# Optimization experiments

Hardware: AMD Instinct MI355X
Metric: run time of the kernel (lower is better)

Reference implementation:

```python
import jax, jax.numpy as jnp
import numpy as np

B, S, I, H, F1, C = 1024, 512, 50, 64, 32, 2


def setup_inputs() -> dict:
    key = jax.random.key(0)
    ks = jax.random.split(key, 9)
    s_ih = 1.0 / np.sqrt(H)
    return {
        "x": jax.random.normal(ks[0], (B, S, I), dtype=jnp.float32),
        # PyTorch LSTM params, gate order (i, f, g, o) stacked along dim 0
        "W_ih": jax.random.uniform(ks[1], (4 * H, I), jnp.float32, -s_ih, s_ih),
        "W_hh": jax.random.uniform(ks[2], (4 * H, H), jnp.float32, -s_ih, s_ih),
        "b_ih": jax.random.uniform(ks[3], (4 * H,), jnp.float32, -s_ih, s_ih),
        "b_hh": jax.random.uniform(ks[4], (4 * H,), jnp.float32, -s_ih, s_ih),
        "W1": jax.random.uniform(ks[5], (F1, H), jnp.float32, -s_ih, s_ih),
        "b1": jax.random.uniform(ks[6], (F1,), jnp.float32, -s_ih, s_ih),
        "W2": jax.random.uniform(ks[7], (C, F1), jnp.float32, -1.0 / np.sqrt(F1), 1.0 / np.sqrt(F1)),
        "b2": jax.random.uniform(ks[8], (C,), jnp.float32, -1.0 / np.sqrt(F1), 1.0 / np.sqrt(F1)),
    }


def _lstm_last(x, W_ih, W_hh, b_ih, b_hh):
    # Precompute input contribution for all timesteps in one big GEMM: [B,S,4H]
    xg = jnp.einsum("bsi,gi->bsg", x, W_ih) + b_ih + b_hh
    Bn = x.shape[0]
    Hn = W_hh.shape[1]
    h0 = jnp.zeros((Bn, Hn), dtype=x.dtype)
    c0 = jnp.zeros((Bn, Hn), dtype=x.dtype)

    def step(carry, xt):
        h, c = carry
        g = xt + h @ W_hh.T  # [B,4H]
        i_g, f_g, g_g, o_g = jnp.split(g, 4, axis=-1)
        i_g = jax.nn.sigmoid(i_g)
        f_g = jax.nn.sigmoid(f_g)
        g_g = jnp.tanh(g_g)
        o_g = jax.nn.sigmoid(o_g)
        c_new = f_g * c + i_g * g_g
        h_new = o_g * jnp.tanh(c_new)
        return (h_new, c_new), None

    (h_last, _), _ = jax.lax.scan(step, (h0, c0), xg.transpose(1, 0, 2))
    return h_last  # == out[:, -1, :]


def reference(x, W_ih, W_hh, b_ih, b_hh, W1, b1, W2, b2):
    last_out = _lstm_last(x, W_ih, W_hh, b_ih, b_hh)
    # Dropout is identity in eval mode (deterministic reference)
    h = jax.nn.relu(last_out @ W1.T + b1)
    return h @ W2.T + b2  # [B, num_classes]
```

## Files before the change

kernel.cpp:

```cpp
#include <hip/hip_runtime.h>
#include <math.h>


#define S_LEN  512
#define I_DIM  50
#define H_DIM  64
#define BB     2
#define TC     16
#define NCH    (S_LEN / TC)
#define KROW   40
#define XROW   72
#define XSHALF (BB * TC * XROW)
#define NXE    (BB * TC * I_DIM)
#define F1_DIM 32
#define C_DIM  2

typedef __attribute__((ext_vector_type(8))) _Float16 f16x8;
typedef __attribute__((ext_vector_type(4))) float    f32x4;

__device__ __forceinline__ float fast_rcp(float x) { return __builtin_amdgcn_rcpf(x); }
__device__ __forceinline__ float sigm(float v) { return fast_rcp(1.0f + __expf(-v)); }
__device__ __forceinline__ float tanh_fast(float v) {
    return 1.0f - 2.0f * fast_rcp(__expf(2.0f * v) + 1.0f);
}

#define MFMA16(A, B, C) __builtin_amdgcn_mfma_f32_16x16x32_f16(A, B, C, 0, 0, 0)

#define BAR() do { asm volatile("s_waitcnt lgkmcnt(0)" ::: "memory"); \
                   __builtin_amdgcn_s_barrier(); } while (0)

__global__ __launch_bounds__(512, 4)
void lstm_mfma(const float* __restrict__ x,
               const float* __restrict__ W_ih, const float* __restrict__ W_hh,
               const float* __restrict__ b_ih, const float* __restrict__ b_hh,
               const float* __restrict__ W1,  const float* __restrict__ b1,
               const float* __restrict__ W2,  const float* __restrict__ b2,
               float* __restrict__ out)
{
    __shared__ __align__(16) _Float16 Hst[2][2][16][KROW];
    __shared__ __align__(16) _Float16 Xs[2][BB * TC][XROW];
    __shared__ __align__(16) float    XGb[2][TC][BB][H_DIM][4];
    __shared__ float f1buf[BB][F1_DIM];

    const int u  = threadIdx.x;
    const int w  = u >> 6;
    const int l  = u & 63;
    const int c  = l & 15;
    const int hk = l >> 4;
    const int b0 = blockIdx.x * BB;
    const bool is_scan = (w < 4);
    const int q  = w & 3;
    const f32x4 Z4 = {0.f, 0.f, 0.f, 0.f};

    f16x8 f0h, f1h, f2h, f3h, f4h, f5h, f6h, f7h;
    float bs0 = 0.f, bs1 = 0.f, bs2 = 0.f, bs3 = 0.f;
    float cst = 0.0f;

    f16x8 ga0, ga1;
    f32x4 G0, G1, G2, G3;

    const float *xp0=x,*xp1=x,*xp2=x,*xp3=x,*xp4=x,*xp5=x,*xp6=x;
    int  ld0=0,ld1=0,ld2=0,ld3=0,ld4=0,ld5=0,ld6=0;
    bool v0=false,v1=false,v2=false,v3=false,v4=false,v5=false,v6=false;

    {
        const int base = is_scan ? (16 * w + c) : (16 * q + c);
#define LDF(NM, G, KT) { \
        _Float16 tmp[8]; \
        _Pragma("unroll") \
        for (int j = 0; j < 8; ++j) { \
            const int kq = hk * 8 + j; \
            if (is_scan) { \
                tmp[j] = (_Float16)W_hh[(G * H_DIM + base) * H_DIM + (KT) * 32 + kq]; \
            } else { \
                const int kk = (KT) * 32 + kq; \
                tmp[j] = (kk < I_DIM) ? (_Float16)W_ih[(G * H_DIM + base) * I_DIM + kk] \
                                      : (_Float16)0.0f; \
            } \
        } \
        NM = *(const f16x8*)tmp; }
        LDF(f0h, 0, 0) LDF(f1h, 0, 1)
        LDF(f2h, 1, 0) LDF(f3h, 1, 1)
        LDF(f4h, 2, 0) LDF(f5h, 2, 1)
        LDF(f6h, 3, 0) LDF(f7h, 3, 1)
#undef LDF
        if (!is_scan) {
            bs0 = b_ih[0 * H_DIM + base] + b_hh[0 * H_DIM + base];
            bs1 = b_ih[1 * H_DIM + base] + b_hh[1 * H_DIM + base];
            bs2 = b_ih[2 * H_DIM + base] + b_hh[2 * H_DIM + base];
            bs3 = b_ih[3 * H_DIM + base] + b_hh[3 * H_DIM + base];

            const int ug = u - 256;
#define PRE(E) { const int idx = ug + (E) * 256; if (idx < NXE) { \
            const int bb_ = idx / (TC * I_DIM); \
            const int rm_ = idx - bb_ * (TC * I_DIM); \
            const int t_  = rm_ / I_DIM; \
            const int ii_ = rm_ - t_ * I_DIM; \
            xp##E = x + (size_t)(b0 + bb_) * (S_LEN * I_DIM) + t_ * I_DIM + ii_; \
            ld##E = (bb_ * TC + t_) * XROW + ii_; v##E = true; } }
            PRE(0) PRE(1) PRE(2) PRE(3) PRE(4) PRE(5) PRE(6)
#undef PRE
        }
    }

    for (int i = u; i < 1280; i += 512) ((unsigned*)Hst)[i] = 0u;
    for (int i = u; i < 2304; i += 512) ((unsigned*)Xs)[i]  = 0u;
    __syncthreads();

    if (!is_scan) {
#define STG(E, CH, BUF) if (v##E) { \
        const float t_ = xp##E[(size_t)(CH) * (TC * I_DIM)]; \
        *((_Float16*)Xs + (BUF) * XSHALF + ld##E) = (_Float16)t_; }
        STG(0,0,0) STG(1,0,0) STG(2,0,0) STG(3,0,0) STG(4,0,0) STG(5,0,0) STG(6,0,0)
        STG(0,1,1) STG(1,1,1) STG(2,1,1) STG(3,1,1) STG(4,1,1) STG(5,1,1) STG(6,1,1)
#undef STG
    }
    __syncthreads();

#define GPK(DB, MT, I) { f32x4 pk; \
    pk[0] = G0[I] + bs0; \
    pk[1] = G1[I] + bs1; \
    pk[2] = G2[I] + bs2; \
    pk[3] = G3[I] + bs3; \
    *(f32x4*)&XGb[DB][4 * hk + (I)][MT][16 * q + c][0] = pk; }

#define GQ0(SB, MT) { \
    ga0 = *(const f16x8*)&Xs[SB][(MT) * 16 + c][hk * 8]; \
    ga1 = *(const f16x8*)&Xs[SB][(MT) * 16 + c][32 + hk * 8]; \
    G0 = MFMA16(ga0, f0h, Z4); G0 = MFMA16(ga1, f1h, G0); }
#define GQ1() { \
    G1 = MFMA16(ga0, f2h, Z4); G1 = MFMA16(ga1, f3h, G1); }
#define GQ2() { \
    G2 = MFMA16(ga0, f4h, Z4); G2 = MFMA16(ga1, f5h, G2); }
#define GQ3(DB, MT) { \
    G3 = MFMA16(ga0, f6h, Z4); G3 = MFMA16(ga1, f7h, G3); \
    GPK(DB, MT, 0) GPK(DB, MT, 1) GPK(DB, MT, 2) GPK(DB, MT, 3) }

    if (!is_scan) {
        GQ0(0, 0) GQ1() GQ2() GQ3(0, 0)
        GQ0(0, 1) GQ1() GQ2() GQ3(0, 1)
    }
    __syncthreads();

#define SCAN_STEP(TT, CUR) { \
    const int p = (TT) & 1; \
    const f16x8 ah0 = *(const f16x8*)&Hst[p][0][c][hk * 8]; \
    const f16x8 ah1 = *(const f16x8*)&Hst[p][1][c][hk * 8]; \
    const int bq = hk & 1; \
    const f32x4 xg4 = *(const f32x4*)&XGb[CUR][TT][bq][16 * w + c][0]; \
    __builtin_amdgcn_s_setprio(1); \
    f32x4 A0 = MFMA16(ah0, f0h, ((f32x4){xg4[0], 0.f, 0.f, 0.f})); \
    A0 = MFMA16(ah1, f1h, A0); \
    f32x4 A1 = MFMA16(ah0, f2h, ((f32x4){xg4[1], 0.f, 0.f, 0.f})); \
    A1 = MFMA16(ah1, f3h, A1); \
    f32x4 A2 = MFMA16(ah0, f4h, ((f32x4){xg4[2], 0.f, 0.f, 0.f})); \
    A2 = MFMA16(ah1, f5h, A2); \
    f32x4 A3 = MFMA16(ah0, f6h, ((f32x4){xg4[3], 0.f, 0.f, 0.f})); \
    A3 = MFMA16(ah1, f7h, A3); \
    __builtin_amdgcn_s_setprio(0); \
    if (hk < 2) { \
        const float gi = sigm(A0[0]), gf = sigm(A1[0]); \
        const float gg = tanh_fast(A2[0]), go = sigm(A3[0]); \
        cst = fmaf(gf, cst, gi * gg); \
        const float hv = go * tanh_fast(cst); \
        const int uo = 16 * w + c; \
        Hst[p ^ 1][uo >> 5][4 * hk][uo & 31] = (_Float16)hv; \
    } }

#define XISS(E, CH2) if (v##E) xr##E = xp##E[(size_t)(CH2) * (TC * I_DIM)];
#define XCMT(E, BUF) if (v##E) *((_Float16*)Xs + (BUF) * XSHALF + ld##E) = (_Float16)xr##E;

    for (int ch = 0; ch < NCH; ++ch) {
        const int cur = ch & 1, nx = cur ^ 1;
        const bool cmp = (ch + 1 < NCH);
        const bool stg = (ch + 2 < NCH);
        float xr0=0,xr1=0,xr2=0,xr3=0,xr4=0,xr5=0,xr6=0;

        #pragma unroll
        for (int tt = 0; tt < TC; ++tt) {
            if (is_scan) {
                SCAN_STEP(tt, cur)
            } else {
                if (cmp && ((tt & 1) == 0)) {
                    const int mt = tt >> 3, gq = (tt >> 1) & 3;
                    if (gq == 0) { GQ0(nx, mt) }
                    if (gq == 1) { GQ1() }
                    if (gq == 2) { GQ2() }
                    if (gq == 3) { GQ3(nx, mt) }
                }
                if (stg) {
                    if (tt == 0) {
                        XISS(0, ch+2) XISS(1, ch+2) XISS(2, ch+2) XISS(3, ch+2)
                        XISS(4, ch+2) XISS(5, ch+2) XISS(6, ch+2)
                    }
                    if (tt == 6)  { XCMT(0, cur)  XCMT(1, cur) }
                    if (tt == 7)  { XCMT(2, cur)  XCMT(3, cur) }
                    if (tt == 9)  { XCMT(4, cur)  XCMT(5, cur) }
                    if (tt == 11) { XCMT(6, cur) }
                }
            }
            BAR();
        }
    }
#undef SCAN_STEP
#undef GQ0
#undef GQ1
#undef GQ2
#undef GQ3
#undef GPK
#undef XISS
#undef XCMT

    __syncthreads();

    if (u < BB * F1_DIM) {
        const int b = u >> 5, f = u & 31;
        float acc = b1[f];
        #pragma unroll
        for (int j = 0; j < H_DIM; ++j) {
            const float hj = (float)Hst[0][j >> 5][4 * b][j & 31];
            acc = fmaf(hj, W1[f * H_DIM + j], acc);
        }
        f1buf[b][f] = fmaxf(acc, 0.0f);
    }
    __syncthreads();
    if (u < BB * C_DIM) {
        const int b = u >> 1, cl = u & 1;
        float acc = b2[cl];
        #pragma unroll
        for (int f = 0; f < F1_DIM; ++f)
            acc = fmaf(f1buf[b][f], W2[cl * F1_DIM + f], acc);
        out[(size_t)(b0 + b) * C_DIM + cl] = acc;
    }
}

extern "C" void kernel_launch(void* const* d_in, const int* in_sizes, int n_in,
                              void* d_out, int out_size, void* d_ws, size_t ws_size,
                              hipStream_t stream) {
    const float* x   = (const float*)d_in[0];
    const float* Wih = (const float*)d_in[1];
    const float* Whh = (const float*)d_in[2];
    const float* bih = (const float*)d_in[3];
    const float* bhh = (const float*)d_in[4];
    const float* W1  = (const float*)d_in[5];
    const float* b1  = (const float*)d_in[6];
    const float* W2  = (const float*)d_in[7];
    const float* b2  = (const float*)d_in[8];
    float* out = (float*)d_out;

    hipLaunchKernelGGL(lstm_mfma, dim3(1024 / BB), dim3(512), 0, stream,
                       x, Wih, Whh, bih, bhh, W1, b1, W2, b2, out);
}
```

Baseline: 221.0 us.

## Merge scan and input-projection warps into one role, process four sequences per block

Removes the producer/consumer split where four warps ran the recurrence and four computed the input projection. Each of the four warps in a 256-thread block now does both, interleaving one input-projection MFMA pair per timestep with the recurrent step. Each block now handles four batch rows instead of two, so each scan MFMA row carries a real sequence. The goal is to halve the block count and use MFMA rows that previously held padding, at the cost of more registers per thread (both weight sets), lower occupancy, and a longer per-step critical path.

```diff
diff --git a/kernel.cpp b/kernel.cpp
--- a/kernel.cpp
+++ b/kernel.cpp
@@ -5,7 +5,7 @@
 #define S_LEN  512
 #define I_DIM  50
 #define H_DIM  64
-#define BB     2
+#define BB     4
 #define TC     16
 #define NCH    (S_LEN / TC)
 #define KROW   40
@@ -29,7 +29,7 @@
 #define BAR() do { asm volatile("s_waitcnt lgkmcnt(0)" ::: "memory"); \
                    __builtin_amdgcn_s_barrier(); } while (0)
 
-__global__ __launch_bounds__(512, 4)
+__global__ __launch_bounds__(256, 1)
 void lstm_mfma(const float* __restrict__ x,
                const float* __restrict__ W_ih, const float* __restrict__ W_hh,
                const float* __restrict__ b_ih, const float* __restrict__ b_hh,
@@ -48,73 +48,66 @@
     const int c  = l & 15;
     const int hk = l >> 4;
     const int b0 = blockIdx.x * BB;
-    const bool is_scan = (w < 4);
-    const int q  = w & 3;
+    const int base = 16 * w + c;
     const f32x4 Z4 = {0.f, 0.f, 0.f, 0.f};
 
-    f16x8 f0h, f1h, f2h, f3h, f4h, f5h, f6h, f7h;
-    float bs0 = 0.f, bs1 = 0.f, bs2 = 0.f, bs3 = 0.f;
+    f16x8 s00, s01, s10, s11, s20, s21, s30, s31;
+    f16x8 g00, g01, g10, g11, g20, g21, g30, g31;
+    {
+#define LDS_F(NM, G, KT) { _Float16 tmp[8]; \
+        _Pragma("unroll") for (int j = 0; j < 8; ++j) \
+            tmp[j] = (_Float16)W_hh[((G) * H_DIM + base) * H_DIM + (KT) * 32 + hk * 8 + j]; \
+        NM = *(const f16x8*)tmp; }
+#define LDG_F(NM, G, KT) { _Float16 tmp[8]; \
+        _Pragma("unroll") for (int j = 0; j < 8; ++j) { \
+            const int kk = (KT) * 32 + hk * 8 + j; \
+            tmp[j] = (kk < I_DIM) ? (_Float16)W_ih[((G) * H_DIM + base) * I_DIM + kk] \
+                                  : (_Float16)0.0f; } \
+        NM = *(const f16x8*)tmp; }
+        LDS_F(s00, 0, 0) LDS_F(s01, 0, 1) LDS_F(s10, 1, 0) LDS_F(s11, 1, 1)
+        LDS_F(s20, 2, 0) LDS_F(s21, 2, 1) LDS_F(s30, 3, 0) LDS_F(s31, 3, 1)
+        LDG_F(g00, 0, 0) LDG_F(g01, 0, 1) LDG_F(g10, 1, 0) LDG_F(g11, 1, 1)
+        LDG_F(g20, 2, 0) LDG_F(g21, 2, 1) LDG_F(g30, 3, 0) LDG_F(g31, 3, 1)
+#undef LDS_F
+#undef LDG_F
+    }
+    const float bs0 = b_ih[0 * H_DIM + base] + b_hh[0 * H_DIM + base];
+    const float bs1 = b_ih[1 * H_DIM + base] + b_hh[1 * H_DIM + base];
+    const float bs2 = b_ih[2 * H_DIM + base] + b_hh[2 * H_DIM + base];
+    const float bs3 = b_ih[3 * H_DIM + base] + b_hh[3 * H_DIM + base];
     float cst = 0.0f;
 
     f16x8 ga0, ga1;
     f32x4 G0, G1, G2, G3;
 
-    const float *xp0=x,*xp1=x,*xp2=x,*xp3=x,*xp4=x,*xp5=x,*xp6=x;
-    int  ld0=0,ld1=0,ld2=0,ld3=0,ld4=0,ld5=0,ld6=0;
-    bool v0=false,v1=false,v2=false,v3=false,v4=false,v5=false,v6=false;
-
-    {
-        const int base = is_scan ? (16 * w + c) : (16 * q + c);
-#define LDF(NM, G, KT) { \
-        _Float16 tmp[8]; \
-        _Pragma("unroll") \
-        for (int j = 0; j < 8; ++j) { \
-            const int kq = hk * 8 + j; \
-            if (is_scan) { \
-                tmp[j] = (_Float16)W_hh[(G * H_DIM + base) * H_DIM + (KT) * 32 + kq]; \
-            } else { \
-                const int kk = (KT) * 32 + kq; \
-                tmp[j] = (kk < I_DIM) ? (_Float16)W_ih[(G * H_DIM + base) * I_DIM + kk] \
-                                      : (_Float16)0.0f; \
-            } \
-        } \
-        NM = *(const f16x8*)tmp; }
-        LDF(f0h, 0, 0) LDF(f1h, 0, 1)
-        LDF(f2h, 1, 0) LDF(f3h, 1, 1)
-        LDF(f4h, 2, 0) LDF(f5h, 2, 1)
-        LDF(f6h, 3, 0) LDF(f7h, 3, 1)
-#undef LDF
-        if (!is_scan) {
-            bs0 = b_ih[0 * H_DIM + base] + b_hh[0 * H_DIM + base];
-            bs1 = b_ih[1 * H_DIM + base] + b_hh[1 * H_DIM + base];
-            bs2 = b_ih[2 * H_DIM + base] + b_hh[2 * H_DIM + base];
-            bs3 = b_ih[3 * H_DIM + base] + b_hh[3 * H_DIM + base];
-
-            const int ug = u - 256;
-#define PRE(E) { const int idx = ug + (E) * 256; if (idx < NXE) { \
-            const int bb_ = idx / (TC * I_DIM); \
-            const int rm_ = idx - bb_ * (TC * I_DIM); \
-            const int t_  = rm_ / I_DIM; \
-            const int ii_ = rm_ - t_ * I_DIM; \
-            xp##E = x + (size_t)(b0 + bb_) * (S_LEN * I_DIM) + t_ * I_DIM + ii_; \
-            ld##E = (bb_ * TC + t_) * XROW + ii_; v##E = true; } }
-            PRE(0) PRE(1) PRE(2) PRE(3) PRE(4) PRE(5) PRE(6)
+    const float *xp0=x,*xp1=x,*xp2=x,*xp3=x,*xp4=x,*xp5=x,*xp6=x,
+                *xp7=x,*xp8=x,*xp9=x,*xp10=x,*xp11=x,*xp12=x;
+    int  ld0=0,ld1=0,ld2=0,ld3=0,ld4=0,ld5=0,ld6=0,ld7=0,ld8=0,ld9=0,ld10=0,ld11=0,ld12=0;
+    bool v0=false,v1=false,v2=false,v3=false,v4=false,v5=false,v6=false,
+         v7=false,v8=false,v9=false,v10=false,v11=false,v12=false;
+#define PRE(E) { const int idx = u + (E) * 256; if (idx < NXE) { \
+        const int bb_ = idx / (TC * I_DIM); \
+        const int rm_ = idx - bb_ * (TC * I_DIM); \
+        const int t_  = rm_ / I_DIM; \
+        const int ii_ = rm_ - t_ * I_DIM; \
+        xp##E = x + (size_t)(b0 + bb_) * (S_LEN * I_DIM) + t_ * I_DIM + ii_; \
+        ld##E = (bb_ * TC + t_) * XROW + ii_; v##E = true; } }
+    PRE(0) PRE(1) PRE(2) PRE(3) PRE(4) PRE(5) PRE(6)
+    PRE(7) PRE(8) PRE(9) PRE(10) PRE(11) PRE(12)
 #undef PRE
-        }
-    }
-
-    for (int i = u; i < 1280; i += 512) ((unsigned*)Hst)[i] = 0u;
-    for (int i = u; i < 2304; i += 512) ((unsigned*)Xs)[i]  = 0u;
-    __syncthreads();
-
-    if (!is_scan) {
+
+    for (int i = u; i < 1280; i += 256) ((unsigned*)Hst)[i] = 0u;
+    for (int i = u; i < 4608; i += 256) ((unsigned*)Xs)[i]  = 0u;
+    __syncthreads();
+
 #define STG(E, CH, BUF) if (v##E) { \
-        const float t_ = xp##E[(size_t)(CH) * (TC * I_DIM)]; \
-        *((_Float16*)Xs + (BUF) * XSHALF + ld##E) = (_Float16)t_; }
-        STG(0,0,0) STG(1,0,0) STG(2,0,0) STG(3,0,0) STG(4,0,0) STG(5,0,0) STG(6,0,0)
-        STG(0,1,1) STG(1,1,1) STG(2,1,1) STG(3,1,1) STG(4,1,1) STG(5,1,1) STG(6,1,1)
+    const float t_ = xp##E[(size_t)(CH) * (TC * I_DIM)]; \
+    *((_Float16*)Xs + (BUF) * XSHALF + ld##E) = (_Float16)t_; }
+    STG(0,0,0) STG(1,0,0) STG(2,0,0) STG(3,0,0) STG(4,0,0) STG(5,0,0) STG(6,0,0)
+    STG(7,0,0) STG(8,0,0) STG(9,0,0) STG(10,0,0) STG(11,0,0) STG(12,0,0)
+    STG(0,1,1) STG(1,1,1) STG(2,1,1) STG(3,1,1) STG(4,1,1) STG(5,1,1) STG(6,1,1)
+    STG(7,1,1) STG(8,1,1) STG(9,1,1) STG(10,1,1) STG(11,1,1) STG(12,1,1)
 #undef STG
-    }
     __syncthreads();
 
 #define GPK(DB, MT, I) { f32x4 pk; \
@@ -122,50 +115,25 @@
     pk[1] = G1[I] + bs1; \
     pk[2] = G2[I] + bs2; \
     pk[3] = G3[I] + bs3; \
-    *(f32x4*)&XGb[DB][4 * hk + (I)][MT][16 * q + c][0] = pk; }
+    *(f32x4*)&XGb[DB][4 * hk + (I)][MT][base][0] = pk; }
 
 #define GQ0(SB, MT) { \
     ga0 = *(const f16x8*)&Xs[SB][(MT) * 16 + c][hk * 8]; \
     ga1 = *(const f16x8*)&Xs[SB][(MT) * 16 + c][32 + hk * 8]; \
-    G0 = MFMA16(ga0, f0h, Z4); G0 = MFMA16(ga1, f1h, G0); }
+    G0 = MFMA16(ga0, g00, Z4); G0 = MFMA16(ga1, g01, G0); }
 #define GQ1() { \
-    G1 = MFMA16(ga0, f2h, Z4); G1 = MFMA16(ga1, f3h, G1); }
+    G1 = MFMA16(ga0, g10, Z4); G1 = MFMA16(ga1, g11, G1); }
 #define GQ2() { \
-    G2 = MFMA16(ga0, f4h, Z4); G2 = MFMA16(ga1, f5h, G2); }
+    G2 = MFMA16(ga0, g20, Z4); G2 = MFMA16(ga1, g21, G2); }
 #define GQ3(DB, MT) { \
-    G3 = MFMA16(ga0, f6h, Z4); G3 = MFMA16(ga1, f7h, G3); \
+    G3 = MFMA16(ga0, g30, Z4); G3 = MFMA16(ga1, g31, G3); \
     GPK(DB, MT, 0) GPK(DB, MT, 1) GPK(DB, MT, 2) GPK(DB, MT, 3) }
 
-    if (!is_scan) {
-        GQ0(0, 0) GQ1() GQ2() GQ3(0, 0)
-        GQ0(0, 1) GQ1() GQ2() GQ3(0, 1)
-    }
-    __syncthreads();
-
-#define SCAN_STEP(TT, CUR) { \
-    const int p = (TT) & 1; \
-    const f16x8 ah0 = *(const f16x8*)&Hst[p][0][c][hk * 8]; \
-    const f16x8 ah1 = *(const f16x8*)&Hst[p][1][c][hk * 8]; \
-    const int bq = hk & 1; \
-    const f32x4 xg4 = *(const f32x4*)&XGb[CUR][TT][bq][16 * w + c][0]; \
-    __builtin_amdgcn_s_setprio(1); \
-    f32x4 A0 = MFMA16(ah0, f0h, ((f32x4){xg4[0], 0.f, 0.f, 0.f})); \
-    A0 = MFMA16(ah1, f1h, A0); \
-    f32x4 A1 = MFMA16(ah0, f2h, ((f32x4){xg4[1], 0.f, 0.f, 0.f})); \
-    A1 = MFMA16(ah1, f3h, A1); \
-    f32x4 A2 = MFMA16(ah0, f4h, ((f32x4){xg4[2], 0.f, 0.f, 0.f})); \
-    A2 = MFMA16(ah1, f5h, A2); \
-    f32x4 A3 = MFMA16(ah0, f6h, ((f32x4){xg4[3], 0.f, 0.f, 0.f})); \
-    A3 = MFMA16(ah1, f7h, A3); \
-    __builtin_amdgcn_s_setprio(0); \
-    if (hk < 2) { \
-        const float gi = sigm(A0[0]), gf = sigm(A1[0]); \
-        const float gg = tanh_fast(A2[0]), go = sigm(A3[0]); \
-        cst = fmaf(gf, cst, gi * gg); \
-        const float hv = go * tanh_fast(cst); \
-        const int uo = 16 * w + c; \
-        Hst[p ^ 1][uo >> 5][4 * hk][uo & 31] = (_Float16)hv; \
-    } }
+    GQ0(0, 0) GQ1() GQ2() GQ3(0, 0)
+    GQ0(0, 1) GQ1() GQ2() GQ3(0, 1)
+    GQ0(0, 2) GQ1() GQ2() GQ3(0, 2)
+    GQ0(0, 3) GQ1() GQ2() GQ3(0, 3)
+    __syncthreads();
 
 #define XISS(E, CH2) if (v##E) xr##E = xp##E[(size_t)(CH2) * (TC * I_DIM)];
 #define XCMT(E, BUF) if (v##E) *((_Float16*)Xs + (BUF) * XSHALF + ld##E) = (_Float16)xr##E;
@@ -174,35 +142,58 @@
         const int cur = ch & 1, nx = cur ^ 1;
         const bool cmp = (ch + 1 < NCH);
         const bool stg = (ch + 2 < NCH);
-        float xr0=0,xr1=0,xr2=0,xr3=0,xr4=0,xr5=0,xr6=0;
+        float xr0=0,xr1=0,xr2=0,xr3=0,xr4=0,xr5=0,xr6=0,
+              xr7=0,xr8=0,xr9=0,xr10=0,xr11=0,xr12=0;
 
         #pragma unroll
         for (int tt = 0; tt < TC; ++tt) {
-            if (is_scan) {
-                SCAN_STEP(tt, cur)
-            } else {
-                if (cmp && ((tt & 1) == 0)) {
-                    const int mt = tt >> 3, gq = (tt >> 1) & 3;
-                    if (gq == 0) { GQ0(nx, mt) }
-                    if (gq == 1) { GQ1() }
-                    if (gq == 2) { GQ2() }
-                    if (gq == 3) { GQ3(nx, mt) }
+            const int p = tt & 1;
+            const f16x8 ah0 = *(const f16x8*)&Hst[p][0][c][hk * 8];
+            const f16x8 ah1 = *(const f16x8*)&Hst[p][1][c][hk * 8];
+            const f32x4 xg4 = *(const f32x4*)&XGb[cur][tt][hk][base][0];
+
+            if (cmp) {
+                const int mt = tt >> 2, gq = tt & 3;
+                if (gq == 0) { GQ0(nx, mt) }
+                if (gq == 1) { GQ1() }
+                if (gq == 2) { GQ2() }
+                if (gq == 3) { GQ3(nx, mt) }
+            }
+            if (stg) {
+                if (tt == 0) {
+                    XISS(0, ch+2) XISS(1, ch+2) XISS(2, ch+2) XISS(3, ch+2)
+                    XISS(4, ch+2) XISS(5, ch+2) XISS(6, ch+2) XISS(7, ch+2)
+                    XISS(8, ch+2) XISS(9, ch+2) XISS(10, ch+2) XISS(11, ch+2)
+                    XISS(12, ch+2)
                 }
-                if (stg) {
-                    if (tt == 0) {
-                        XISS(0, ch+2) XISS(1, ch+2) XISS(2, ch+2) XISS(3, ch+2)
-                        XISS(4, ch+2) XISS(5, ch+2) XISS(6, ch+2)
-                    }
-                    if (tt == 6)  { XCMT(0, cur)  XCMT(1, cur) }
-                    if (tt == 7)  { XCMT(2, cur)  XCMT(3, cur) }
-                    if (tt == 9)  { XCMT(4, cur)  XCMT(5, cur) }
-                    if (tt == 11) { XCMT(6, cur) }
-                }
+                if (tt == 6)  { XCMT(0, cur)  XCMT(1, cur) }
+                if (tt == 7)  { XCMT(2, cur)  XCMT(3, cur) }
+                if (tt == 8)  { XCMT(4, cur)  XCMT(5, cur) }
+                if (tt == 9)  { XCMT(6, cur)  XCMT(7, cur) }
+                if (tt == 10) { XCMT(8, cur)  XCMT(9, cur) }
+                if (tt == 11) { XCMT(10, cur) XCMT(11, cur) }
+                if (tt == 12) { XCMT(12, cur) }
+            }
+
+            f32x4 A0 = MFMA16(ah0, s00, ((f32x4){xg4[0], 0.f, 0.f, 0.f}));
+            A0 = MFMA16(ah1, s01, A0);
+            f32x4 A1 = MFMA16(ah0, s10, ((f32x4){xg4[1], 0.f, 0.f, 0.f}));
+            A1 = MFMA16(ah1, s11, A1);
+            f32x4 A2 = MFMA16(ah0, s20, ((f32x4){xg4[2], 0.f, 0.f, 0.f}));
+            A2 = MFMA16(ah1, s21, A2);
+            f32x4 A3 = MFMA16(ah0, s30, ((f32x4){xg4[3], 0.f, 0.f, 0.f}));
+            A3 = MFMA16(ah1, s31, A3);
+
+            {
+                const float gi = sigm(A0[0]), gf = sigm(A1[0]);
+                const float gg = tanh_fast(A2[0]), go = sigm(A3[0]);
+                cst = fmaf(gf, cst, gi * gg);
+                const float hv = go * tanh_fast(cst);
+                Hst[p ^ 1][base >> 5][4 * hk][base & 31] = (_Float16)hv;
             }
             BAR();
         }
     }
-#undef SCAN_STEP
 #undef GQ0
 #undef GQ1
 #undef GQ2
@@ -248,6 +239,6 @@
     const float* b2  = (const float*)d_in[8];
     float* out = (float*)d_out;
 
-    hipLaunchKernelGGL(lstm_mfma, dim3(1024 / BB), dim3(512), 0, stream,
+    hipLaunchKernelGGL(lstm_mfma, dim3(1024 / BB), dim3(256), 0, stream,
                        x, Wih, Whh, bih, bhh, W1, b1, W2, b2, out);
 }
```

New measurement: 192.8 us. -12.8%, faster.
